# Optimization experiments

Measured on AMD Instinct MI355X. Metric: run time of the kernel, lower is better.

## Reference

```python
import jax, jax.numpy as jnp
import numpy as np

C, D, K, N, R = 96, 192, 4, 16, 6  # d_model, d_inner, directions, d_state, dt_rank
B, H, W = 8, 64, 64


def _ln(x, w, b):
    mu = x.mean(-1, keepdims=True)
    var = ((x - mu) ** 2).mean(-1, keepdims=True)
    return (x - mu) * jax.lax.rsqrt(var + 1e-5) * w + b


def setup_inputs() -> dict:
    key = jax.random.key(0)
    ks = jax.random.split(key, 16)
    s = 0.02
    A = jnp.tile(jnp.arange(1, N + 1, dtype=jnp.float32)[None, None, :], (K, D, 1))
    return {
        "x": jax.random.normal(ks[0], (B, C, H, W), jnp.float32),
        "ln1_w": jnp.ones((C,), jnp.float32),
        "ln1_b": jnp.zeros((C,), jnp.float32),
        "in_proj_w": jax.random.normal(ks[1], (2 * D, C), jnp.float32) * s,
        "conv_w": jax.random.normal(ks[2], (D, 1, 3, 3), jnp.float32) * s,
        "conv_b": jnp.zeros((D,), jnp.float32),
        "x_proj_w": jax.random.normal(ks[3], (K, R + 2 * N, D), jnp.float32) * s,
        "dt_projs_w": jax.random.normal(ks[4], (K, D, R), jnp.float32) * s,
        "dt_projs_b": jax.random.normal(ks[5], (K, D), jnp.float32) * 0.1,
        "A_logs": jnp.log(A),
        "Ds": jnp.ones((K, D), jnp.float32),
        "out_norm_w": jnp.ones((D,), jnp.float32),
        "out_norm_b": jnp.zeros((D,), jnp.float32),
        "out_proj_w": jax.random.normal(ks[6], (C, D), jnp.float32) * s,
        "pm_norm_w": jnp.ones((4 * C,), jnp.float32),
        "pm_norm_b": jnp.zeros((4 * C,), jnp.float32),
        "pm_red_w": jax.random.normal(ks[7], (2 * C, 4 * C), jnp.float32) * s,
    }


def reference(x, ln1_w, ln1_b, in_proj_w, conv_w, conv_b, x_proj_w, dt_projs_w,
              dt_projs_b, A_logs, Ds, out_norm_w, out_norm_b, out_proj_w,
              pm_norm_w, pm_norm_b, pm_red_w):
    b, c, h, w = x.shape
    L = h * w
    xh = jnp.transpose(x, (0, 2, 3, 1))  # [B,H,W,C]
    resid = xh
    xn = _ln(xh, ln1_w, ln1_b)
    xz = xn @ in_proj_w.T  # [B,H,W,2D]
    xp, z = xz[..., :D], xz[..., D:]
    xc = jnp.transpose(xp, (0, 3, 1, 2))  # [B,D,H,W]
    xc = jax.lax.conv_general_dilated(
        xc, conv_w, (1, 1), ((1, 1), (1, 1)),
        dimension_numbers=("NCHW", "OIHW", "NCHW"), feature_group_count=D)
    xc = jax.nn.silu(xc + conv_b[None, :, None, None])
    # cross-scan: row-major, col-major, and their reverses -> [B,K,D,L]
    xf = xc.reshape(b, D, L)
    xt = jnp.transpose(xc, (0, 1, 3, 2)).reshape(b, D, L)
    xs = jnp.stack([xf, xt, xf[..., ::-1], xt[..., ::-1]], axis=1)
    x_dbl = jnp.einsum("bkdl,kcd->bkcl", xs, x_proj_w)
    dts = jnp.einsum("bkrl,kdr->bkdl", x_dbl[:, :, :R], dt_projs_w)
    Bs = x_dbl[:, :, R:R + N]  # [B,K,N,L]
    Cs = x_dbl[:, :, R + N:R + 2 * N]
    delta = jax.nn.softplus(dts + dt_projs_b[None, :, :, None])  # [B,K,D,L]
    A = -jnp.exp(A_logs)  # [K,D,N]
    dT = jnp.transpose(delta, (3, 0, 1, 2))  # [L,B,K,D]
    uT = jnp.transpose(xs, (3, 0, 1, 2))
    BT = jnp.transpose(Bs, (3, 0, 1, 2))  # [L,B,K,N]
    CT = jnp.transpose(Cs, (3, 0, 1, 2))
    h0 = jnp.zeros((b, K, D, N), x.dtype)

    def step(hst, inp):
        dt, ut, bt, ct = inp
        hst = hst * jnp.exp(dt[..., None] * A) + (dt * ut)[..., None] * bt[:, :, None, :]
        return hst, jnp.einsum("bkdn,bkn->bkd", hst, ct)

    _, yT = jax.lax.scan(step, h0, (dT, uT, BT, CT))  # yT: [L,B,K,D]
    y = jnp.transpose(yT, (1, 2, 3, 0)) + Ds[None, :, :, None] * xs  # [B,K,D,L]

    def unT(v):  # undo col-major traversal
        return jnp.transpose(v.reshape(b, D, w, h), (0, 1, 3, 2)).reshape(b, D, L)

    yc = y[:, 0] + y[:, 2, :, ::-1] + unT(y[:, 1]) + unT(y[:, 3, :, ::-1])
    yo = jnp.transpose(yc.reshape(b, D, h, w), (0, 2, 3, 1))  # [B,H,W,D]
    yo = _ln(yo, out_norm_w, out_norm_b) * jax.nn.silu(z)
    out = resid + yo @ out_proj_w.T  # [B,H,W,C]
    # PatchMerging2D
    x0 = out[:, 0::2, 0::2]
    x1 = out[:, 1::2, 0::2]
    x2 = out[:, 0::2, 1::2]
    x3 = out[:, 1::2, 1::2]
    xm = jnp.concatenate([x0, x1, x2, x3], -1)  # [B,H/2,W/2,4C]
    xm = _ln(xm, pm_norm_w, pm_norm_b) @ pm_red_w.T  # [B,H/2,W/2,2C]
    return jnp.transpose(xm, (0, 3, 1, 2))
```

## Files before the change

kernel.cpp:

```cpp
#include <hip/hip_runtime.h>
#include <hip/hip_bf16.h>


__device__ __forceinline__ float sigm(float x){ return 1.f/(1.f+__expf(-x)); }
__device__ __forceinline__ float softplus_(float x){ return (x>20.f)? x : __logf(1.f+__expf(x)); }

__device__ __forceinline__ void scan_p0dp(int k, int ch, int& p0, int& dp){
  switch(k){
    case 0:  p0 = ch*64;        dp = 1;   break;
    case 1:  p0 = ch;           dp = 64;  break;
    case 2:  p0 = 4095 - ch*64; dp = -1;  break;
    default: p0 = 4095 - ch;    dp = -64; break;
  }
}

__global__ __launch_bounds__(256) void k0_prep(
    const float* __restrict__ ipw, const float* __restrict__ xpw,
    const float* __restrict__ dtw, const float* __restrict__ opw,
    const float* __restrict__ pmw,
    float* __restrict__ ipwT, float* __restrict__ xpwTp,
    float* __restrict__ dtwT, float* __restrict__ opwT,
    float* __restrict__ pmwT)
{
  int g = blockIdx.x*256 + threadIdx.x;
  if(g < 36864){
    int c = g/384, n = g%384;
    ipwT[g] = ipw[n*96 + c];
  } else if(g < 67584){
    int t = g - 36864; int dd = t/160, n = t - dd*160; int k = n/40, c = n - k*40;
    float v;
    if(c < 6)       v = xpw[(k*38 + c)*192 + dd];
    else if(c < 8)  v = 0.f;
    else            v = xpw[(k*38 + (c-2))*192 + dd];
    xpwTp[t] = v;
  } else if(g < 72192){
    int t = g - 67584; int kr = t/192, d = t - kr*192; int k = kr/6, r = kr - k*6;
    dtwT[t] = dtw[(k*192 + d)*6 + r];
  } else if(g < 90624){
    int t = g - 72192; int d = t/96, c = t - d*96;
    opwT[t] = opw[c*192 + d];
  } else if(g < 164352){
    int t = g - 90624; int n = t/192, c2 = t - n*192;
    pmwT[t] = pmw[c2*384 + n];
  }
}

#define XT_PAD 68
__global__ __launch_bounds__(256) void k1_ln_inproj(
    const float* __restrict__ x, const float* __restrict__ lnw, const float* __restrict__ lnb,
    const float* __restrict__ ipwT, float* __restrict__ xT,
    float* __restrict__ xp, float* __restrict__ z)
{
  __shared__ float xt[96*XT_PAD];
  __shared__ float lnw_s[96], lnb_s[96], mu_s[64], rs_s[64];
  int tid = threadIdx.x;
  int mt = blockIdx.x, nt = blockIdx.y, b = blockIdx.z;
  int g0 = mt*64;
  const float* xb = x + (size_t)b*96*4096 + g0;
  for(int idx=tid; idx<6144; idx+=256){
    int c = idx>>6, p = idx&63;
    xt[c*XT_PAD+p] = xb[c*4096 + p];
  }
  if(tid<96){ lnw_s[tid]=lnw[tid]; lnb_s[tid]=lnb[tid]; }
  __syncthreads();
  if(nt==0){
    float* xTb = xT + ((size_t)(b*4096 + g0))*96;
    for(int idx=tid; idx<6144; idx+=256){
      int p = idx/96, c = idx - p*96;
      xTb[idx] = xt[c*XT_PAD+p];
    }
  }
  if(tid<64){
    float s=0.f,q=0.f;
    for(int c=0;c<96;c++){ float v=xt[c*XT_PAD+tid]; s+=v; q+=v*v; }
    float mu = s*(1.f/96.f);
    mu_s[tid]=mu; rs_s[tid]=rsqrtf(q*(1.f/96.f)-mu*mu+1e-5f);
  }
  __syncthreads();
  for(int idx=tid; idx<6144; idx+=256){
    int c = idx>>6, p = idx&63;
    int a = c*XT_PAD+p;
    xt[a] = (xt[a]-mu_s[p])*rs_s[p]*lnw_s[c]+lnb_s[c];
  }
  __syncthreads();
  int tm = tid>>5, tn = tid&31;
  float acc[8][4];
  #pragma unroll
  for(int i=0;i<8;i++){acc[i][0]=0.f;acc[i][1]=0.f;acc[i][2]=0.f;acc[i][3]=0.f;}
  const float* wbase = ipwT + nt*128 + tn*4;
  for(int kk=0;kk<96;kk++){
    float4 w4 = *(const float4*)(wbase + kk*384);
    float4 a0 = *(const float4*)&xt[kk*XT_PAD + tm*8];
    float4 a1 = *(const float4*)&xt[kk*XT_PAD + tm*8 + 4];
    float av[8]={a0.x,a0.y,a0.z,a0.w,a1.x,a1.y,a1.z,a1.w};
    #pragma unroll
    for(int i=0;i<8;i++){
      acc[i][0]=fmaf(av[i],w4.x,acc[i][0]);
      acc[i][1]=fmaf(av[i],w4.y,acc[i][1]);
      acc[i][2]=fmaf(av[i],w4.z,acc[i][2]);
      acc[i][3]=fmaf(av[i],w4.w,acc[i][3]);
    }
  }
  int n = nt*128 + tn*4;
  #pragma unroll
  for(int i=0;i<8;i++){
    size_t row = (size_t)(b*4096 + g0 + tm*8 + i);
    float4 v = make_float4(acc[i][0],acc[i][1],acc[i][2],acc[i][3]);
    if(n < 192) *(float4*)(xp + row*192 + n) = v;
    else        *(float4*)(z  + row*192 + (n-192)) = v;
  }
}

__global__ __launch_bounds__(192) void k2_conv(
    const float* __restrict__ xp, const float* __restrict__ cw, const float* __restrict__ cb,
    float* __restrict__ xc)
{
  __shared__ float cw_s[1728];
  int tid = threadIdx.x;
  int pq = blockIdx.x, b = blockIdx.y;
  for(int i=tid;i<1728;i+=192) cw_s[i]=cw[i];
  __syncthreads();
  int p0 = pq*4;
  int h = p0>>6, w0 = p0&63;
  const float* base = xp + (size_t)b*4096*192 + tid;
  const float* wp = &cw_s[tid*9];
  float bias = cb[tid];
  float acc[4] = {bias,bias,bias,bias};
  #pragma unroll
  for(int ky=0;ky<3;ky++){
    int hh = h+ky-1;
    if(hh<0||hh>63) continue;
    float v[6];
    #pragma unroll
    for(int xx=0;xx<6;xx++){
      int ww = w0-1+xx;
      v[xx] = (ww>=0 && ww<64) ? base[((size_t)(hh*64+ww))*192] : 0.f;
    }
    float wk0=wp[ky*3], wk1=wp[ky*3+1], wk2=wp[ky*3+2];
    #pragma unroll
    for(int j=0;j<4;j++)
      acc[j] = fmaf(v[j],wk0, fmaf(v[j+1],wk1, fmaf(v[j+2],wk2, acc[j])));
  }
  #pragma unroll
  for(int j=0;j<4;j++){
    float a = acc[j];
    a = a * sigm(a);
    xc[((size_t)(b*4096)+p0+j)*192 + tid] = a;
  }
}

__global__ __launch_bounds__(320) void k3_proj(
    const float* __restrict__ xc, const float* __restrict__ xpwTp,
    float* __restrict__ xdbl)
{
  __shared__ float sm[32*192];
  int tid = threadIdx.x;
  int mt = blockIdx.x, b = blockIdx.y;
  int g0 = mt*32;
  const float* xcb = xc + ((size_t)(b*4096 + g0))*192;
  for(int idx=tid; idx<6144; idx+=320) sm[idx] = xcb[idx];
  __syncthreads();
  int tn = tid%40, tm = tid/40;
  float acc[4][4];
  #pragma unroll
  for(int i=0;i<4;i++){acc[i][0]=0.f;acc[i][1]=0.f;acc[i][2]=0.f;acc[i][3]=0.f;}
  const float* wb = xpwTp + tn*4;
  for(int kk=0;kk<192;kk+=2){
    float4 w0 = *(const float4*)(wb + kk*160);
    float4 w1 = *(const float4*)(wb + (kk+1)*160);
    #pragma unroll
    for(int i=0;i<4;i++){
      float2 a = *(const float2*)&sm[(tm*4+i)*192 + kk];
      acc[i][0] = fmaf(a.x,w0.x, fmaf(a.y,w1.x, acc[i][0]));
      acc[i][1] = fmaf(a.x,w0.y, fmaf(a.y,w1.y, acc[i][1]));
      acc[i][2] = fmaf(a.x,w0.z, fmaf(a.y,w1.z, acc[i][2]));
      acc[i][3] = fmaf(a.x,w0.w, fmaf(a.y,w1.w, acc[i][3]));
    }
  }
  #pragma unroll
  for(int i=0;i<4;i++){
    *(float4*)(xdbl + ((size_t)(b*4096 + g0 + tm*4 + i))*160 + tn*4)
      = make_float4(acc[i][0],acc[i][1],acc[i][2],acc[i][3]);
  }
}

__global__ __launch_bounds__(192) void k4a_scanlocal(
    const float* __restrict__ xdbl, const float* __restrict__ xc,
    const float* __restrict__ alog, const float* __restrict__ dtwT,
    const float* __restrict__ dtb,
    float* __restrict__ localH, float* __restrict__ decayT)
{
  __shared__ float rows[64*40];
  int d = threadIdx.x;
  int ch = blockIdx.x, k = blockIdx.y, b = blockIdx.z;
  size_t prow = (size_t)b*4096;
  int p0, dp;
  scan_p0dp(k, ch, p0, dp);
  for(int idx4=d; idx4<640; idx4+=192){
    int i = idx4/10, c4 = idx4 - i*10;
    *(float4*)&rows[idx4*4] =
      *(const float4*)(xdbl + (prow + (size_t)(p0 + i*dp))*160 + k*40 + c4*4);
  }
  float w0=dtwT[(k*6+0)*192+d], w1=dtwT[(k*6+1)*192+d], w2=dtwT[(k*6+2)*192+d],
        w3=dtwT[(k*6+3)*192+d], w4=dtwT[(k*6+4)*192+d], w5=dtwT[(k*6+5)*192+d];
  float dtbv = dtb[k*192+d];
  float A0; bool fast = true;
  {
    const float4* ap = (const float4*)(alog + (size_t)(k*192+d)*16);
    float4 a0=ap[0],a1=ap[1],a2=ap[2],a3=ap[3];
    float t[16]={a0.x,a0.y,a0.z,a0.w,a1.x,a1.y,a1.z,a1.w,a2.x,a2.y,a2.z,a2.w,a3.x,a3.y,a3.z,a3.w};
    A0 = -__expf(t[0]);
    #pragma unroll
    for(int n=1;n<16;n++)
      fast = fast && (fabsf(-__expf(t[n]) - (float)(n+1)*A0) <= 1e-4f*(float)(n+1)*fabsf(A0));
  }
  float h[16];
  #pragma unroll
  for(int n=0;n<16;n++) h[n]=0.f;
  float S=0.f;
  const float* xu = xc + (prow + (size_t)p0)*192 + d;
  ptrdiff_t ustride = (ptrdiff_t)dp*192;
  float dec[16];
  __syncthreads();
  if(fast){
    for(int i=0;i<64;i++){
      const float* row = &rows[i*40];
      float u = *xu; xu += ustride;
      float p01 = fmaf(row[1],w1, row[0]*w0);
      float p23 = fmaf(row[3],w3, row[2]*w2);
      float p45 = fmaf(row[5],w5, row[4]*w4);
      float delta = softplus_((dtbv + p01) + (p23 + p45));
      float du = delta*u;
      S += delta;
      float4 B0=*(const float4*)(row+8),  B1=*(const float4*)(row+12),
             B2=*(const float4*)(row+16), B3=*(const float4*)(row+20);
      float e1=__expf(delta*A0);
      float e2=e1*e1;
      float c0=e1, c1=e2, c2=e2*e1, e4=e2*e2, c3=e4;
      h[0]=fmaf(h[0],c0,du*B0.x); h[1]=fmaf(h[1],c1,du*B0.y);
      h[2]=fmaf(h[2],c2,du*B0.z); h[3]=fmaf(h[3],c3,du*B0.w);
      c0*=e4; c1*=e4; c2*=e4; c3*=e4;
      h[4]=fmaf(h[4],c0,du*B1.x); h[5]=fmaf(h[5],c1,du*B1.y);
      h[6]=fmaf(h[6],c2,du*B1.z); h[7]=fmaf(h[7],c3,du*B1.w);
      c0*=e4; c1*=e4; c2*=e4; c3*=e4;
      h[8]=fmaf(h[8],c0,du*B2.x); h[9]=fmaf(h[9],c1,du*B2.y);
      h[10]=fmaf(h[10],c2,du*B2.z); h[11]=fmaf(h[11],c3,du*B2.w);
      c0*=e4; c1*=e4; c2*=e4; c3*=e4;
      h[12]=fmaf(h[12],c0,du*B3.x); h[13]=fmaf(h[13],c1,du*B3.y);
      h[14]=fmaf(h[14],c2,du*B3.z); h[15]=fmaf(h[15],c3,du*B3.w);
    }
    float s1=__expf(S*A0);
    float s2=s1*s1;
    float c0=s1, c1=s2, c2=s2*s1, s4=s2*s2, c3=s4;
    dec[0]=c0; dec[1]=c1; dec[2]=c2; dec[3]=c3;
    c0*=s4; c1*=s4; c2*=s4; c3*=s4;
    dec[4]=c0; dec[5]=c1; dec[6]=c2; dec[7]=c3;
    c0*=s4; c1*=s4; c2*=s4; c3*=s4;
    dec[8]=c0; dec[9]=c1; dec[10]=c2; dec[11]=c3;
    c0*=s4; c1*=s4; c2*=s4; c3*=s4;
    dec[12]=c0; dec[13]=c1; dec[14]=c2; dec[15]=c3;
  } else {
    float A[16];
    {
      const float4* ap = (const float4*)(alog + (size_t)(k*192+d)*16);
      float4 a0=ap[0],a1=ap[1],a2=ap[2],a3=ap[3];
      float t[16]={a0.x,a0.y,a0.z,a0.w,a1.x,a1.y,a1.z,a1.w,a2.x,a2.y,a2.z,a2.w,a3.x,a3.y,a3.z,a3.w};
      #pragma unroll
      for(int n=0;n<16;n++) A[n] = -__expf(t[n]);
    }
    for(int i=0;i<64;i++){
      const float* row = &rows[i*40];
      float u = *xu; xu += ustride;
      float p01 = fmaf(row[1],w1, row[0]*w0);
      float p23 = fmaf(row[3],w3, row[2]*w2);
      float p45 = fmaf(row[5],w5, row[4]*w4);
      float delta = softplus_((dtbv + p01) + (p23 + p45));
      float du = delta*u;
      S += delta;
      float4 B0=*(const float4*)(row+8),  B1=*(const float4*)(row+12),
             B2=*(const float4*)(row+16), B3=*(const float4*)(row+20);
      float Bn[16]={B0.x,B0.y,B0.z,B0.w,B1.x,B1.y,B1.z,B1.w,
                    B2.x,B2.y,B2.z,B2.w,B3.x,B3.y,B3.z,B3.w};
      #pragma unroll
      for(int n=0;n<16;n++) h[n] = fmaf(h[n], __expf(delta*A[n]), du*Bn[n]);
    }
    #pragma unroll
    for(int n=0;n<16;n++) dec[n] = __expf(A[n]*S);
  }
  float* lh = localH + ((((size_t)(b*4+k))*64 + ch)*192 + d)*16;
  float* dt = decayT + ((((size_t)(b*4+k))*64 + ch)*192 + d)*16;
  #pragma unroll
  for(int n4=0;n4<4;n4++){
    *(float4*)(lh + n4*4) = make_float4(h[n4*4],h[n4*4+1],h[n4*4+2],h[n4*4+3]);
    *(float4*)(dt + n4*4) = make_float4(dec[n4*4],dec[n4*4+1],dec[n4*4+2],dec[n4*4+3]);
  }
}

__global__ __launch_bounds__(256) void k4b_chain(
    float* __restrict__ localH, const float* __restrict__ decayT)
{
  int g = blockIdx.x*256 + threadIdx.x;
  int bk = g/3072, dn = g - bk*3072;
  float hv = 0.f;
  size_t base = (size_t)bk*64*3072 + dn;
  for(int ch=0; ch<64; ch++){
    size_t idx = base + (size_t)ch*3072;
    float loc = localH[idx], dec = decayT[idx];
    localH[idx] = hv;
    hv = fmaf(hv, dec, loc);
  }
}

__global__ __launch_bounds__(192) void k4c_scanfull(
    const float* __restrict__ xdbl, const float* __restrict__ xc,
    const float* __restrict__ alog, const float* __restrict__ dtwT,
    const float* __restrict__ dtb, const float* __restrict__ hin,
    const float* __restrict__ Dsv, float* __restrict__ yB)
{
  __shared__ float rows[64*40];
  int d = threadIdx.x;
  int ch = blockIdx.x, k = blockIdx.y, b = blockIdx.z;
  size_t prow = (size_t)b*4096;
  int p0, dp;
  scan_p0dp(k, ch, p0, dp);
  for(int idx4=d; idx4<640; idx4+=192){
    int i = idx4/10, c4 = idx4 - i*10;
    *(float4*)&rows[idx4*4] =
      *(const float4*)(xdbl + (prow + (size_t)(p0 + i*dp))*160 + k*40 + c4*4);
  }
  float w0=dtwT[(k*6+0)*192+d], w1=dtwT[(k*6+1)*192+d], w2=dtwT[(k*6+2)*192+d],
        w3=dtwT[(k*6+3)*192+d], w4=dtwT[(k*6+4)*192+d], w5=dtwT[(k*6+5)*192+d];
  float dtbv = dtb[k*192+d];
  float A0; bool fast = true;
  {
    const float4* ap = (const float4*)(alog + (size_t)(k*192+d)*16);
    float4 a0=ap[0],a1=ap[1],a2=ap[2],a3=ap[3];
    float t[16]={a0.x,a0.y,a0.z,a0.w,a1.x,a1.y,a1.z,a1.w,a2.x,a2.y,a2.z,a2.w,a3.x,a3.y,a3.z,a3.w};
    A0 = -__expf(t[0]);
    #pragma unroll
    for(int n=1;n<16;n++)
      fast = fast && (fabsf(-__expf(t[n]) - (float)(n+1)*A0) <= 1e-4f*(float)(n+1)*fabsf(A0));
  }
  float h[16];
  {
    const float4* hp = (const float4*)(hin + ((((size_t)(b*4+k))*64 + ch)*192 + d)*16);
    float4 h0=hp[0],h1=hp[1],h2=hp[2],h3=hp[3];
    h[0]=h0.x;h[1]=h0.y;h[2]=h0.z;h[3]=h0.w;h[4]=h1.x;h[5]=h1.y;h[6]=h1.z;h[7]=h1.w;
    h[8]=h2.x;h[9]=h2.y;h[10]=h2.z;h[11]=h2.w;h[12]=h3.x;h[13]=h3.y;h[14]=h3.z;h[15]=h3.w;
  }
  float dsv = Dsv[k*192+d];
  const float* xu = xc + (prow + (size_t)p0)*192 + d;
  ptrdiff_t ustride = (ptrdiff_t)dp*192;
  float* yP = yB + (((size_t)(b*4+k))*4096 + ch*64)*192 + d;
  __syncthreads();
  if(fast){
    for(int i=0;i<64;i++){
      const float* row = &rows[i*40];
      float u = *xu; xu += ustride;
      float p01 = fmaf(row[1],w1, row[0]*w0);
      float p23 = fmaf(row[3],w3, row[2]*w2);
      float p45 = fmaf(row[5],w5, row[4]*w4);
      float delta = softplus_((dtbv + p01) + (p23 + p45));
      float du = delta*u;
      float4 B0=*(const float4*)(row+8),  B1=*(const float4*)(row+12),
             B2=*(const float4*)(row+16), B3=*(const float4*)(row+20);
      float4 C0=*(const float4*)(row+24), C1=*(const float4*)(row+28),
             C2=*(const float4*)(row+32), C3=*(const float4*)(row+36);
      float e1=__expf(delta*A0);
      float e2=e1*e1;
      float c0=e1, c1=e2, c2=e2*e1, e4=e2*e2, c3=e4;
      h[0]=fmaf(h[0],c0,du*B0.x); h[1]=fmaf(h[1],c1,du*B0.y);
      h[2]=fmaf(h[2],c2,du*B0.z); h[3]=fmaf(h[3],c3,du*B0.w);
      float y0 = fmaf(h[0],C0.x, fmaf(h[1],C0.y, fmaf(h[2],C0.z, h[3]*C0.w)));
      c0*=e4; c1*=e4; c2*=e4; c3*=e4;
      h[4]=fmaf(h[4],c0,du*B1.x); h[5]=fmaf(h[5],c1,du*B1.y);
      h[6]=fmaf(h[6],c2,du*B1.z); h[7]=fmaf(h[7],c3,du*B1.w);
      float y1 = fmaf(h[4],C1.x, fmaf(h[5],C1.y, fmaf(h[6],C1.z, h[7]*C1.w)));
      c0*=e4; c1*=e4; c2*=e4; c3*=e4;
      h[8]=fmaf(h[8],c0,du*B2.x); h[9]=fmaf(h[9],c1,du*B2.y);
      h[10]=fmaf(h[10],c2,du*B2.z); h[11]=fmaf(h[11],c3,du*B2.w);
      float y2 = fmaf(h[8],C2.x, fmaf(h[9],C2.y, fmaf(h[10],C2.z, h[11]*C2.w)));
      c0*=e4; c1*=e4; c2*=e4; c3*=e4;
      h[12]=fmaf(h[12],c0,du*B3.x); h[13]=fmaf(h[13],c1,du*B3.y);
      h[14]=fmaf(h[14],c2,du*B3.z); h[15]=fmaf(h[15],c3,du*B3.w);
      float y3 = fmaf(h[12],C3.x, fmaf(h[13],C3.y, fmaf(h[14],C3.z, h[15]*C3.w)));
      yP[(size_t)i*192] = fmaf(dsv, u, (y0+y1)+(y2+y3));
    }
  } else {
    float A[16];
    {
      const float4* ap = (const float4*)(alog + (size_t)(k*192+d)*16);
      float4 a0=ap[0],a1=ap[1],a2=ap[2],a3=ap[3];
      float t[16]={a0.x,a0.y,a0.z,a0.w,a1.x,a1.y,a1.z,a1.w,a2.x,a2.y,a2.z,a2.w,a3.x,a3.y,a3.z,a3.w};
      #pragma unroll
      for(int n=0;n<16;n++) A[n] = -__expf(t[n]);
    }
    for(int i=0;i<64;i++){
      const float* row = &rows[i*40];
      float u = *xu; xu += ustride;
      float p01 = fmaf(row[1],w1, row[0]*w0);
      float p23 = fmaf(row[3],w3, row[2]*w2);
      float p45 = fmaf(row[5],w5, row[4]*w4);
      float delta = softplus_((dtbv + p01) + (p23 + p45));
      float du = delta*u;
      float4 B0=*(const float4*)(row+8),  B1=*(const float4*)(row+12),
             B2=*(const float4*)(row+16), B3=*(const float4*)(row+20);
      float Bn[16]={B0.x,B0.y,B0.z,B0.w,B1.x,B1.y,B1.z,B1.w,
                    B2.x,B2.y,B2.z,B2.w,B3.x,B3.y,B3.z,B3.w};
      float4 C0=*(const float4*)(row+24), C1=*(const float4*)(row+28),
             C2=*(const float4*)(row+32), C3=*(const float4*)(row+36);
      float Cn[16]={C0.x,C0.y,C0.z,C0.w,C1.x,C1.y,C1.z,C1.w,
                    C2.x,C2.y,C2.z,C2.w,C3.x,C3.y,C3.z,C3.w};
      float y = 0.f;
      #pragma unroll
      for(int n=0;n<16;n++){
        h[n] = fmaf(h[n], __expf(delta*A[n]), du*Bn[n]);
        y = fmaf(h[n], Cn[n], y);
      }
      yP[(size_t)i*192] = fmaf(dsv, u, y);
    }
  }
}

#define YPAD 193
__global__ __launch_bounds__(256) void k5_combine(
    const float* __restrict__ yS, const float* __restrict__ z, const float* __restrict__ xT,
    const float* __restrict__ onw, const float* __restrict__ onb,
    const float* __restrict__ opwT, float* __restrict__ out_pre)
{
  __shared__ float yn[64*YPAD];
  __shared__ float wsm[48*96];
  __shared__ float mu_s[64], rs_s[64];
  int tid = threadIdx.x;
  int mt = blockIdx.x, b = blockIdx.y;
  int g0 = mt*64;
  size_t base = (size_t)b*4*4096;
  for(int idx=tid; idx<12288; idx+=256){
    int p = idx/192, d = idx - p*192;
    int gp = g0 + p;
    int l1 = ((gp&63)<<6)|(gp>>6);
    float v = yS[(base + gp)*192 + d]
            + yS[(base + 4096 + l1)*192 + d]
            + yS[(base + 2*4096 + (4095-gp))*192 + d]
            + yS[(base + 3*4096 + (4095-l1))*192 + d];
    yn[p*YPAD+d] = v;
  }
  __syncthreads();
  {
    int p = tid>>2, q = tid&3;
    float s=0.f, sq=0.f;
    for(int c=q;c<192;c+=4){ float v=yn[p*YPAD+c]; s+=v; sq=fmaf(v,v,sq); }
    s  += __shfl_xor(s,1);  sq += __shfl_xor(sq,1);
    s  += __shfl_xor(s,2);  sq += __shfl_xor(sq,2);
    if(q==0){
      float mu = s*(1.f/192.f);
      mu_s[p]=mu; rs_s[p]=rsqrtf(sq*(1.f/192.f)-mu*mu+1e-5f);
    }
  }
  __syncthreads();
  for(int idx=tid; idx<12288; idx+=256){
    int p = idx/192, d = idx - p*192;
    float zz = z[((size_t)(b*4096+g0+p))*192 + d];
    float v = (yn[p*YPAD+d]-mu_s[p])*rs_s[p]*onw[d]+onb[d];
    yn[p*YPAD+d] = v * zz * sigm(zz);
  }
  __syncthreads();
  int tn = tid&15, tm = tid>>4;
  float acc[4][6];
  #pragma unroll
  for(int i=0;i<4;i++)
    #pragma unroll
    for(int j=0;j<6;j++) acc[i][j]=0.f;
  for(int kc=0; kc<4; kc++){
    for(int idx=tid; idx<4608; idx+=256) wsm[idx] = opwT[kc*4608 + idx];
    __syncthreads();
    for(int kk=0;kk<48;kk++){
      float a0 = yn[(tm*4+0)*YPAD + kc*48+kk];
      float a1 = yn[(tm*4+1)*YPAD + kc*48+kk];
      float a2 = yn[(tm*4+2)*YPAD + kc*48+kk];
      float a3 = yn[(tm*4+3)*YPAD + kc*48+kk];
      const float* wr = &wsm[kk*96 + tn*6];
      #pragma unroll
      for(int j=0;j<6;j++){
        float w = wr[j];
        acc[0][j]=fmaf(a0,w,acc[0][j]);
        acc[1][j]=fmaf(a1,w,acc[1][j]);
        acc[2][j]=fmaf(a2,w,acc[2][j]);
        acc[3][j]=fmaf(a3,w,acc[3][j]);
      }
    }
    __syncthreads();
  }
  #pragma unroll
  for(int i=0;i<4;i++){
    size_t row = (size_t)(b*4096 + g0 + tm*4 + i);
    const float* xr = xT + row*96 + tn*6;
    float* orr = out_pre + row*96 + tn*6;
    #pragma unroll
    for(int j=0;j<6;j++) orr[j] = acc[i][j] + xr[j];
  }
}

__global__ __launch_bounds__(192) void k6_pm(
    const float* __restrict__ out_pre, const float* __restrict__ pmw, const float* __restrict__ pmb,
    const float* __restrict__ pmwT, float* __restrict__ outp)
{
  __shared__ float xm[8*388];
  __shared__ float xo[8*193];
  __shared__ float mus[8], rss[8];
  int tid = threadIdx.x;
  int jt = blockIdx.x, i = blockIdx.y, b = blockIdx.z;
  for(int idx=tid; idx<3072; idx+=192){
    int pj = idx/384, n = idx - pj*384;
    int q = n/96, c = n - q*96;
    int j = jt*8 + pj;
    int h2 = 2*i + (q&1), w2 = 2*j + (q>>1);
    xm[pj*388+n] = out_pre[((size_t)b*4096 + h2*64 + w2)*96 + c];
  }
  __syncthreads();
  if(tid<8){
    float s=0.f,q=0.f;
    for(int n=0;n<384;n++){ float v=xm[tid*388+n]; s+=v; q+=v*v; }
    float mu=s*(1.f/384.f);
    mus[tid]=mu; rss[tid]=rsqrtf(q*(1.f/384.f)-mu*mu+1e-5f);
  }
  __syncthreads();
  for(int idx=tid; idx<3072; idx+=192){
    int pj = idx/384, n = idx - pj*384;
    xm[pj*388+n] = (xm[pj*388+n]-mus[pj])*rss[pj]*pmw[n]+pmb[n];
  }
  __syncthreads();
  float acc[8];
  #pragma unroll
  for(int pj=0;pj<8;pj++) acc[pj]=0.f;
  const float* wb = pmwT + tid;
  for(int n4=0;n4<96;n4++){
    float w0=wb[(n4*4+0)*192], w1=wb[(n4*4+1)*192], w2=wb[(n4*4+2)*192], w3=wb[(n4*4+3)*192];
    #pragma unroll
    for(int pj=0;pj<8;pj++){
      float4 v = *(const float4*)&xm[pj*388 + n4*4];
      acc[pj] = fmaf(v.x,w0,fmaf(v.y,w1,fmaf(v.z,w2,fmaf(v.w,w3,acc[pj]))));
    }
  }
  #pragma unroll
  for(int pj=0;pj<8;pj++) xo[pj*193+tid]=acc[pj];
  __syncthreads();
  for(int idx=tid; idx<1536; idx+=192){
    int c2 = idx>>3, pj = idx&7;
    outp[(((size_t)b*192 + c2)*32 + i)*32 + jt*8 + pj] = xo[pj*193+c2];
  }
}

extern "C" void kernel_launch(void* const* d_in, const int* in_sizes, int n_in,
                              void* d_out, int out_size, void* d_ws, size_t ws_size,
                              hipStream_t stream)
{
  const float* x    = (const float*)d_in[0];
  const float* lnw  = (const float*)d_in[1];
  const float* lnb  = (const float*)d_in[2];
  const float* ipw  = (const float*)d_in[3];
  const float* cw   = (const float*)d_in[4];
  const float* cb   = (const float*)d_in[5];
  const float* xpw  = (const float*)d_in[6];
  const float* dtw  = (const float*)d_in[7];
  const float* dtb  = (const float*)d_in[8];
  const float* alog = (const float*)d_in[9];
  const float* Dsv  = (const float*)d_in[10];
  const float* onw  = (const float*)d_in[11];
  const float* onb  = (const float*)d_in[12];
  const float* opw  = (const float*)d_in[13];
  const float* pmnw = (const float*)d_in[14];
  const float* pmnb = (const float*)d_in[15];
  const float* pmrw = (const float*)d_in[16];
  float* out = (float*)d_out;

  float* ws    = (float*)d_ws;
  float* xT    = ws;
  float* xpb   = xT + 3145728;
  float* zb    = xpb + 6291456;
  float* xcb   = zb + 6291456;
  float* yB    = xcb + 6291456;
  float* lH    = yB + 25165824;
  float* dT    = lH + 6291456;
  float* ipwT  = dT + 6291456;
  float* xpwTp = ipwT + 36864;
  float* dtwT  = xpwTp + 30720;
  float* opwT  = dtwT + 4608;
  float* pmwT  = opwT + 18432;
  float* xdbl  = xpb;
  float* outp  = xpb;

  k0_prep      <<<dim3(642),     dim3(256), 0, stream>>>(ipw,xpw,dtw,opw,pmrw, ipwT,xpwTp,dtwT,opwT,pmwT);
  k1_ln_inproj <<<dim3(64,3,8),  dim3(256), 0, stream>>>(x,lnw,lnb,ipwT, xT,xpb,zb);
  k2_conv      <<<dim3(1024,8),  dim3(192), 0, stream>>>(xpb,cw,cb, xcb);
  k3_proj      <<<dim3(128,8),   dim3(320), 0, stream>>>(xcb,xpwTp, xdbl);
  k4a_scanlocal<<<dim3(64,4,8),  dim3(192), 0, stream>>>(xdbl,xcb,alog,dtwT,dtb, lH,dT);
  k4b_chain    <<<dim3(384),     dim3(256), 0, stream>>>(lH,dT);
  k4c_scanfull <<<dim3(64,4,8),  dim3(192), 0, stream>>>(xdbl,xcb,alog,dtwT,dtb,lH,Dsv, yB);
  k5_combine   <<<dim3(64,8),    dim3(256), 0, stream>>>(yB,zb,xT,onw,onb,opwT, outp);
  k6_pm        <<<dim3(4,32,8),  dim3(192), 0, stream>>>(outp,pmnw,pmnb,pmwT, out);
}
```

Before: 351.8 us.

## Split scans into shorter chunks, derive decay from delta sums, retile conv

The chunked selective scan now uses 128 chunks of 32 steps instead of 64 of 64, which doubles the number of scan blocks. The chain pass now recomputes each chunk's decay from a stored per-channel delta sum instead of reading a full per-state decay tensor. When A equals -1..-16 exactly, exp(delta*A0) is computed as 1/(1+exp(raw)), reusing the softplus exponential, and the dt-projection inputs are read with vector loads. The depthwise conv now computes 2x8 output tiles per thread so neighbouring input rows are reused. In exchange the local-state buffer and the serial chain length double, and the fast path is specialised to the exact A_log values the test inputs use.

```diff
diff --git a/kernel.cpp b/kernel.cpp
--- a/kernel.cpp
+++ b/kernel.cpp
@@ -2,16 +2,17 @@
 #include <hip/hip_bf16.h>
 
 
+#define NCH 128
+#define CLEN 32
+
 __device__ __forceinline__ float sigm(float x){ return 1.f/(1.f+__expf(-x)); }
 __device__ __forceinline__ float softplus_(float x){ return (x>20.f)? x : __logf(1.f+__expf(x)); }
 
-__device__ __forceinline__ void scan_p0dp(int k, int ch, int& p0, int& dp){
-  switch(k){
-    case 0:  p0 = ch*64;        dp = 1;   break;
-    case 1:  p0 = ch;           dp = 64;  break;
-    case 2:  p0 = 4095 - ch*64; dp = -1;  break;
-    default: p0 = 4095 - ch;    dp = -64; break;
-  }
+__device__ __forceinline__ void scan_p0dp2(int k, int v0, int& p0, int& dp){
+  if(k==0){ p0 = v0; dp = 1; }
+  else if(k==1){ p0 = ((v0&63)<<6)|(v0>>6); dp = 64; }
+  else if(k==2){ p0 = 4095 - v0; dp = -1; }
+  else { int m0 = 4095 - v0; p0 = ((m0&63)<<6)|(m0>>6); dp = -64; }
 }
 
 __global__ __launch_bounds__(256) void k0_prep(
@@ -120,33 +121,44 @@
   int pq = blockIdx.x, b = blockIdx.y;
   for(int i=tid;i<1728;i+=192) cw_s[i]=cw[i];
   __syncthreads();
-  int p0 = pq*4;
-  int h = p0>>6, w0 = p0&63;
+  int th = (pq>>3)<<1;
+  int tw = (pq&7)<<3;
   const float* base = xp + (size_t)b*4096*192 + tid;
   const float* wp = &cw_s[tid*9];
   float bias = cb[tid];
-  float acc[4] = {bias,bias,bias,bias};
-  #pragma unroll
-  for(int ky=0;ky<3;ky++){
-    int hh = h+ky-1;
+  float acc[2][8];
+  #pragma unroll
+  for(int r=0;r<2;r++)
+    #pragma unroll
+    for(int j=0;j<8;j++) acc[r][j]=bias;
+  #pragma unroll
+  for(int iy=0; iy<4; iy++){
+    int hh = th-1+iy;
     if(hh<0||hh>63) continue;
-    float v[6];
-    #pragma unroll
-    for(int xx=0;xx<6;xx++){
-      int ww = w0-1+xx;
+    float v[10];
+    #pragma unroll
+    for(int xx=0;xx<10;xx++){
+      int ww = tw-1+xx;
       v[xx] = (ww>=0 && ww<64) ? base[((size_t)(hh*64+ww))*192] : 0.f;
     }
-    float wk0=wp[ky*3], wk1=wp[ky*3+1], wk2=wp[ky*3+2];
-    #pragma unroll
-    for(int j=0;j<4;j++)
-      acc[j] = fmaf(v[j],wk0, fmaf(v[j+1],wk1, fmaf(v[j+2],wk2, acc[j])));
-  }
-  #pragma unroll
-  for(int j=0;j<4;j++){
-    float a = acc[j];
-    a = a * sigm(a);
-    xc[((size_t)(b*4096)+p0+j)*192 + tid] = a;
-  }
+    #pragma unroll
+    for(int r=0;r<2;r++){
+      int ky = iy - r;
+      if(ky<0||ky>2) continue;
+      float wk0=wp[ky*3], wk1=wp[ky*3+1], wk2=wp[ky*3+2];
+      #pragma unroll
+      for(int j=0;j<8;j++)
+        acc[r][j] = fmaf(v[j],wk0, fmaf(v[j+1],wk1, fmaf(v[j+2],wk2, acc[r][j])));
+    }
+  }
+  #pragma unroll
+  for(int r=0;r<2;r++)
+    #pragma unroll
+    for(int j=0;j<8;j++){
+      float a = acc[r][j];
+      a = a * sigm(a);
+      xc[((size_t)(b*4096) + (th+r)*64 + tw+j)*192 + tid] = a;
+    }
 }
 
 __global__ __launch_bounds__(320) void k3_proj(
@@ -188,15 +200,15 @@
     const float* __restrict__ xdbl, const float* __restrict__ xc,
     const float* __restrict__ alog, const float* __restrict__ dtwT,
     const float* __restrict__ dtb,
-    float* __restrict__ localH, float* __restrict__ decayT)
-{
-  __shared__ float rows[64*40];
+    float* __restrict__ localH, float* __restrict__ Ssum)
+{
+  __shared__ float rows[CLEN*40];
   int d = threadIdx.x;
   int ch = blockIdx.x, k = blockIdx.y, b = blockIdx.z;
   size_t prow = (size_t)b*4096;
   int p0, dp;
-  scan_p0dp(k, ch, p0, dp);
-  for(int idx4=d; idx4<640; idx4+=192){
+  scan_p0dp2(k, ch*CLEN, p0, dp);
+  for(int idx4=d; idx4<CLEN*10; idx4+=192){
     int i = idx4/10, c4 = idx4 - i*10;
     *(float4*)&rows[idx4*4] =
       *(const float4*)(xdbl + (prow + (size_t)(p0 + i*dp))*160 + k*40 + c4*4);
@@ -204,15 +216,17 @@
   float w0=dtwT[(k*6+0)*192+d], w1=dtwT[(k*6+1)*192+d], w2=dtwT[(k*6+2)*192+d],
         w3=dtwT[(k*6+3)*192+d], w4=dtwT[(k*6+4)*192+d], w5=dtwT[(k*6+5)*192+d];
   float dtbv = dtb[k*192+d];
-  float A0; bool fast = true;
+  float A0; bool fast1;
   {
     const float4* ap = (const float4*)(alog + (size_t)(k*192+d)*16);
     float4 a0=ap[0],a1=ap[1],a2=ap[2],a3=ap[3];
     float t[16]={a0.x,a0.y,a0.z,a0.w,a1.x,a1.y,a1.z,a1.w,a2.x,a2.y,a2.z,a2.w,a3.x,a3.y,a3.z,a3.w};
     A0 = -__expf(t[0]);
+    bool fast = true;
     #pragma unroll
     for(int n=1;n<16;n++)
       fast = fast && (fabsf(-__expf(t[n]) - (float)(n+1)*A0) <= 1e-4f*(float)(n+1)*fabsf(A0));
+    fast1 = fast && (A0 == -1.0f);
   }
   float h[16];
   #pragma unroll
@@ -220,21 +234,25 @@
   float S=0.f;
   const float* xu = xc + (prow + (size_t)p0)*192 + d;
   ptrdiff_t ustride = (ptrdiff_t)dp*192;
-  float dec[16];
-  __syncthreads();
-  if(fast){
-    for(int i=0;i<64;i++){
+  __syncthreads();
+  if(fast1){
+    for(int i=0;i<CLEN;i++){
       const float* row = &rows[i*40];
       float u = *xu; xu += ustride;
-      float p01 = fmaf(row[1],w1, row[0]*w0);
-      float p23 = fmaf(row[3],w3, row[2]*w2);
-      float p45 = fmaf(row[5],w5, row[4]*w4);
-      float delta = softplus_((dtbv + p01) + (p23 + p45));
+      float4 r03 = *(const float4*)row;
+      float2 r45 = *(const float2*)(row+4);
+      float p01 = fmaf(r03.y,w1, r03.x*w0);
+      float p23 = fmaf(r03.w,w3, r03.z*w2);
+      float p45 = fmaf(r45.y,w5, r45.x*w4);
+      float raw = (dtbv + p01) + (p23 + p45);
+      float ex = __expf(raw);
+      float tt = 1.f + ex;
+      float delta = (raw>20.f)? raw : __logf(tt);
+      float e1 = __builtin_amdgcn_rcpf(tt);
       float du = delta*u;
       S += delta;
       float4 B0=*(const float4*)(row+8),  B1=*(const float4*)(row+12),
              B2=*(const float4*)(row+16), B3=*(const float4*)(row+20);
-      float e1=__expf(delta*A0);
       float e2=e1*e1;
       float c0=e1, c1=e2, c2=e2*e1, e4=e2*e2, c3=e4;
       h[0]=fmaf(h[0],c0,du*B0.x); h[1]=fmaf(h[1],c1,du*B0.y);
@@ -249,16 +267,6 @@
       h[12]=fmaf(h[12],c0,du*B3.x); h[13]=fmaf(h[13],c1,du*B3.y);
       h[14]=fmaf(h[14],c2,du*B3.z); h[15]=fmaf(h[15],c3,du*B3.w);
     }
-    float s1=__expf(S*A0);
-    float s2=s1*s1;
-    float c0=s1, c1=s2, c2=s2*s1, s4=s2*s2, c3=s4;
-    dec[0]=c0; dec[1]=c1; dec[2]=c2; dec[3]=c3;
-    c0*=s4; c1*=s4; c2*=s4; c3*=s4;
-    dec[4]=c0; dec[5]=c1; dec[6]=c2; dec[7]=c3;
-    c0*=s4; c1*=s4; c2*=s4; c3*=s4;
-    dec[8]=c0; dec[9]=c1; dec[10]=c2; dec[11]=c3;
-    c0*=s4; c1*=s4; c2*=s4; c3*=s4;
-    dec[12]=c0; dec[13]=c1; dec[14]=c2; dec[15]=c3;
   } else {
     float A[16];
     {
@@ -268,7 +276,7 @@
       #pragma unroll
       for(int n=0;n<16;n++) A[n] = -__expf(t[n]);
     }
-    for(int i=0;i<64;i++){
+    for(int i=0;i<CLEN;i++){
       const float* row = &rows[i*40];
       float u = *xu; xu += ustride;
       float p01 = fmaf(row[1],w1, row[0]*w0);
@@ -284,29 +292,32 @@
       #pragma unroll
       for(int n=0;n<16;n++) h[n] = fmaf(h[n], __expf(delta*A[n]), du*Bn[n]);
     }
-    #pragma unroll
-    for(int n=0;n<16;n++) dec[n] = __expf(A[n]*S);
-  }
-  float* lh = localH + ((((size_t)(b*4+k))*64 + ch)*192 + d)*16;
-  float* dt = decayT + ((((size_t)(b*4+k))*64 + ch)*192 + d)*16;
-  #pragma unroll
-  for(int n4=0;n4<4;n4++){
+  }
+  float* lh = localH + ((((size_t)(b*4+k))*NCH + ch)*192 + d)*16;
+  #pragma unroll
+  for(int n4=0;n4<4;n4++)
     *(float4*)(lh + n4*4) = make_float4(h[n4*4],h[n4*4+1],h[n4*4+2],h[n4*4+3]);
-    *(float4*)(dt + n4*4) = make_float4(dec[n4*4],dec[n4*4+1],dec[n4*4+2],dec[n4*4+3]);
-  }
+  Ssum[(((size_t)(b*4+k))*NCH + ch)*192 + d] = S;
 }
 
 __global__ __launch_bounds__(256) void k4b_chain(
-    float* __restrict__ localH, const float* __restrict__ decayT)
+    float* __restrict__ localH, const float* __restrict__ Ssum,
+    const float* __restrict__ alog)
 {
   int g = blockIdx.x*256 + threadIdx.x;
   int bk = g/3072, dn = g - bk*3072;
+  int k = bk & 3;
+  int d = dn>>4, n = dn&15;
+  float A = -__expf(alog[((size_t)(k*192+d))*16 + n]);
   float hv = 0.f;
-  size_t base = (size_t)bk*64*3072 + dn;
-  for(int ch=0; ch<64; ch++){
-    size_t idx = base + (size_t)ch*3072;
-    float loc = localH[idx], dec = decayT[idx];
-    localH[idx] = hv;
+  size_t hbase = (size_t)bk*NCH*3072 + dn;
+  size_t sbase = (size_t)bk*NCH*192 + d;
+  for(int ch=0; ch<NCH; ch++){
+    size_t hidx = hbase + (size_t)ch*3072;
+    float loc = localH[hidx];
+    float S = Ssum[sbase + (size_t)ch*192];
+    float dec = __expf(A*S);
+    localH[hidx] = hv;
     hv = fmaf(hv, dec, loc);
   }
 }
@@ -317,13 +328,13 @@
     const float* __restrict__ dtb, const float* __restrict__ hin,
     const float* __restrict__ Dsv, float* __restrict__ yB)
 {
-  __shared__ float rows[64*40];
+  __shared__ float rows[CLEN*40];
   int d = threadIdx.x;
   int ch = blockIdx.x, k = blockIdx.y, b = blockIdx.z;
   size_t prow = (size_t)b*4096;
   int p0, dp;
-  scan_p0dp(k, ch, p0, dp);
-  for(int idx4=d; idx4<640; idx4+=192){
+  scan_p0dp2(k, ch*CLEN, p0, dp);
+  for(int idx4=d; idx4<CLEN*10; idx4+=192){
     int i = idx4/10, c4 = idx4 - i*10;
     *(float4*)&rows[idx4*4] =
       *(const float4*)(xdbl + (prow + (size_t)(p0 + i*dp))*160 + k*40 + c4*4);
@@ -331,19 +342,21 @@
   float w0=dtwT[(k*6+0)*192+d], w1=dtwT[(k*6+1)*192+d], w2=dtwT[(k*6+2)*192+d],
         w3=dtwT[(k*6+3)*192+d], w4=dtwT[(k*6+4)*192+d], w5=dtwT[(k*6+5)*192+d];
   float dtbv = dtb[k*192+d];
-  float A0; bool fast = true;
+  float A0; bool fast1;
   {
     const float4* ap = (const float4*)(alog + (size_t)(k*192+d)*16);
     float4 a0=ap[0],a1=ap[1],a2=ap[2],a3=ap[3];
     float t[16]={a0.x,a0.y,a0.z,a0.w,a1.x,a1.y,a1.z,a1.w,a2.x,a2.y,a2.z,a2.w,a3.x,a3.y,a3.z,a3.w};
     A0 = -__expf(t[0]);
+    bool fast = true;
     #pragma unroll
     for(int n=1;n<16;n++)
       fast = fast && (fabsf(-__expf(t[n]) - (float)(n+1)*A0) <= 1e-4f*(float)(n+1)*fabsf(A0));
+    fast1 = fast && (A0 == -1.0f);
   }
   float h[16];
   {
-    const float4* hp = (const float4*)(hin + ((((size_t)(b*4+k))*64 + ch)*192 + d)*16);
+    const float4* hp = (const float4*)(hin + ((((size_t)(b*4+k))*NCH + ch)*192 + d)*16);
     float4 h0=hp[0],h1=hp[1],h2=hp[2],h3=hp[3];
     h[0]=h0.x;h[1]=h0.y;h[2]=h0.z;h[3]=h0.w;h[4]=h1.x;h[5]=h1.y;h[6]=h1.z;h[7]=h1.w;
     h[8]=h2.x;h[9]=h2.y;h[10]=h2.z;h[11]=h2.w;h[12]=h3.x;h[13]=h3.y;h[14]=h3.z;h[15]=h3.w;
@@ -351,22 +364,27 @@
   float dsv = Dsv[k*192+d];
   const float* xu = xc + (prow + (size_t)p0)*192 + d;
   ptrdiff_t ustride = (ptrdiff_t)dp*192;
-  float* yP = yB + (((size_t)(b*4+k))*4096 + ch*64)*192 + d;
-  __syncthreads();
-  if(fast){
-    for(int i=0;i<64;i++){
+  float* yP = yB + (((size_t)(b*4+k))*4096 + ch*CLEN)*192 + d;
+  __syncthreads();
+  if(fast1){
+    for(int i=0;i<CLEN;i++){
       const float* row = &rows[i*40];
       float u = *xu; xu += ustride;
-      float p01 = fmaf(row[1],w1, row[0]*w0);
-      float p23 = fmaf(row[3],w3, row[2]*w2);
-      float p45 = fmaf(row[5],w5, row[4]*w4);
-      float delta = softplus_((dtbv + p01) + (p23 + p45));
+      float4 r03 = *(const float4*)row;
+      float2 r45 = *(const float2*)(row+4);
+      float p01 = fmaf(r03.y,w1, r03.x*w0);
+      float p23 = fmaf(r03.w,w3, r03.z*w2);
+      float p45 = fmaf(r45.y,w5, r45.x*w4);
+      float raw = (dtbv + p01) + (p23 + p45);
+      float ex = __expf(raw);
+      float tt = 1.f + ex;
+      float delta = (raw>20.f)? raw : __logf(tt);
+      float e1 = __builtin_amdgcn_rcpf(tt);
       float du = delta*u;
       float4 B0=*(const float4*)(row+8),  B1=*(const float4*)(row+12),
              B2=*(const float4*)(row+16), B3=*(const float4*)(row+20);
       float4 C0=*(const float4*)(row+24), C1=*(const float4*)(row+28),
              C2=*(const float4*)(row+32), C3=*(const float4*)(row+36);
-      float e1=__expf(delta*A0);
       float e2=e1*e1;
       float c0=e1, c1=e2, c2=e2*e1, e4=e2*e2, c3=e4;
       h[0]=fmaf(h[0],c0,du*B0.x); h[1]=fmaf(h[1],c1,du*B0.y);
@@ -395,7 +413,7 @@
       #pragma unroll
       for(int n=0;n<16;n++) A[n] = -__expf(t[n]);
     }
-    for(int i=0;i<64;i++){
+    for(int i=0;i<CLEN;i++){
       const float* row = &rows[i*40];
       float u = *xu; xu += ustride;
       float p01 = fmaf(row[1],w1, row[0]*w0);
@@ -581,8 +599,8 @@
   float* xcb   = zb + 6291456;
   float* yB    = xcb + 6291456;
   float* lH    = yB + 25165824;
-  float* dT    = lH + 6291456;
-  float* ipwT  = dT + 6291456;
+  float* Ss    = lH + 12582912;
+  float* ipwT  = Ss + 786432;
   float* xpwTp = ipwT + 36864;
   float* dtwT  = xpwTp + 30720;
   float* opwT  = dtwT + 4608;
@@ -590,13 +608,13 @@
   float* xdbl  = xpb;
   float* outp  = xpb;
 
-  k0_prep      <<<dim3(642),     dim3(256), 0, stream>>>(ipw,xpw,dtw,opw,pmrw, ipwT,xpwTp,dtwT,opwT,pmwT);
-  k1_ln_inproj <<<dim3(64,3,8),  dim3(256), 0, stream>>>(x,lnw,lnb,ipwT, xT,xpb,zb);
-  k2_conv      <<<dim3(1024,8),  dim3(192), 0, stream>>>(xpb,cw,cb, xcb);
-  k3_proj      <<<dim3(128,8),   dim3(320), 0, stream>>>(xcb,xpwTp, xdbl);
-  k4a_scanlocal<<<dim3(64,4,8),  dim3(192), 0, stream>>>(xdbl,xcb,alog,dtwT,dtb, lH,dT);
-  k4b_chain    <<<dim3(384),     dim3(256), 0, stream>>>(lH,dT);
-  k4c_scanfull <<<dim3(64,4,8),  dim3(192), 0, stream>>>(xdbl,xcb,alog,dtwT,dtb,lH,Dsv, yB);
-  k5_combine   <<<dim3(64,8),    dim3(256), 0, stream>>>(yB,zb,xT,onw,onb,opwT, outp);
-  k6_pm        <<<dim3(4,32,8),  dim3(192), 0, stream>>>(outp,pmnw,pmnb,pmwT, out);
-}
+  k0_prep      <<<dim3(642),      dim3(256), 0, stream>>>(ipw,xpw,dtw,opw,pmrw, ipwT,xpwTp,dtwT,opwT,pmwT);
+  k1_ln_inproj <<<dim3(64,3,8),   dim3(256), 0, stream>>>(x,lnw,lnb,ipwT, xT,xpb,zb);
+  k2_conv      <<<dim3(256,8),    dim3(192), 0, stream>>>(xpb,cw,cb, xcb);
+  k3_proj      <<<dim3(128,8),    dim3(320), 0, stream>>>(xcb,xpwTp, xdbl);
+  k4a_scanlocal<<<dim3(NCH,4,8),  dim3(192), 0, stream>>>(xdbl,xcb,alog,dtwT,dtb, lH,Ss);
+  k4b_chain    <<<dim3(384),      dim3(256), 0, stream>>>(lH,Ss,alog);
+  k4c_scanfull <<<dim3(NCH,4,8),  dim3(192), 0, stream>>>(xdbl,xcb,alog,dtwT,dtb,lH,Dsv, yB);
+  k5_combine   <<<dim3(64,8),     dim3(256), 0, stream>>>(yB,zb,xT,onw,onb,opwT, outp);
+  k6_pm        <<<dim3(4,32,8),   dim3(192), 0, stream>>>(outp,pmnw,pmnb,pmwT, out);
+}
```

New measurement: 366.7 us. +4.2%, slower.
